# Kernel optimization log

Measured on AMD Instinct MI355X. Metric: run time of the kernel, lower is better.

Reference implementation:

```python
import jax, jax.numpy as jnp
import numpy as np

B, S = 2048, 8192


def setup_inputs() -> dict:
    key = jax.random.key(0)
    ks = jax.random.split(key, 8)
    X = jax.random.normal(ks[0], (B, S, 4), dtype=jnp.float32)
    # make column 0 a monotonically increasing time grid (seconds)
    t = jnp.broadcast_to(jnp.arange(S, dtype=jnp.float32), (B, S))
    X = X.at[..., 0].set(t)
    SC = jax.random.uniform(ks[1], (B, 4), dtype=jnp.float32, minval=0.5, maxval=1.5)
    W1 = jax.random.normal(ks[2], (1, 4), dtype=jnp.float32) * 0.5
    b1 = jnp.zeros((1,), jnp.float32)
    W2 = jax.random.normal(ks[3], (1, 1), dtype=jnp.float32) * 0.5
    b2 = jnp.zeros((1,), jnp.float32)
    Wa = jax.random.normal(ks[4], (1, 2), dtype=jnp.float32) * 0.5
    ba = jnp.zeros((1,), jnp.float32)
    Wb = jax.random.normal(ks[5], (1, 1), dtype=jnp.float32) * 0.5
    bb = jnp.zeros((1,), jnp.float32)
    return {"X": X, "SC": SC, "W1": W1, "b1": b1, "W2": W2, "b2": b2,
            "Wa": Wa, "ba": ba, "Wb": Wb, "bb": bb}


def reference(X, SC, W1, b1, W2, b2, Wa, ba, Wb, bb):
    # X: [B,S,4] = (t, I, T, U); SC: [B,4] = (Q, eta_0, R, SOC_init_ref)
    I = X[..., 1:2]          # [B,S,1]
    T = X[..., 2:3]
    U = X[..., 3:4]
    R = SC[..., 2:3]         # [B,1]
    # initial-SOC net on first-step features
    init_feats = jnp.concatenate(
        [I[:, 0:1], T[:, 0:1], U[:, 0:1], R[:, None, :]], axis=-1)  # [B,1,4]
    h = jax.nn.softplus(init_feats @ W1.T + b1)
    SOC_init_raw = (h @ W2.T + b2).squeeze(-1)                      # [B,1]
    SOC_init = (SC[..., 3:4] * (1.0 + SOC_init_raw))[:, :, None]    # [B,1,1]
    # efficiency-correction net over whole sequence
    eta_in = jnp.concatenate([I, T], axis=-1)                       # [B,S,2]
    delta_eta = jax.nn.softplus(eta_in @ Wa.T + ba) @ Wb.T + bb     # [B,S,1]
    Q = SC[..., 0:1][:, None, :]     # [B,1,1]
    eta0 = SC[..., 1:2][:, None, :]  # [B,1,1]
    # dSOC/dt does not depend on SOC -> Euler loop == prefix sum
    rate = eta0 * (1.0 + delta_eta) * I / (3600.0 * Q)              # [B,S,1]
    times = X[..., 0]                                               # [B,S]
    dt = (times[:, 1:] - times[:, :-1])[..., None]                  # [B,S-1,1]
    delta_SOC = rate[:, :-1] * dt                                   # [B,S-1,1]
    SOC = jnp.concatenate(
        [SOC_init, SOC_init + jnp.cumsum(delta_SOC, axis=1)], axis=1)  # [B,S,1]
    return SOC
```

## Files before the change

### kernel.cpp

```cpp
#include <hip/hip_runtime.h>


#define BLOCK 1024

__device__ __forceinline__ float softplusf(float x) {
    return fmaxf(x, 0.0f) + log1pf(expf(-fabsf(x)));
}

__global__ __launch_bounds__(BLOCK) void soc_scan_kernel(
    const float* __restrict__ X,
    const float* __restrict__ SC,
    const float* __restrict__ W1, const float* __restrict__ b1,
    const float* __restrict__ W2, const float* __restrict__ b2,
    const float* __restrict__ Wa, const float* __restrict__ ba,
    const float* __restrict__ Wb, const float* __restrict__ bb,
    float* __restrict__ out, const int S)
{
    const int b    = blockIdx.x;
    const int tid  = threadIdx.x;
    const int lane = tid & 63;
    const int wv   = tid >> 6;
    const int NW   = BLOCK >> 6;

    __shared__ float sEdgeRate[16];
    __shared__ float sEdgeT[16];
    __shared__ float sWaveSum[16];
    __shared__ float sWaveOff[16];
    __shared__ float sBlockTot;
    __shared__ float sPrevRate;
    __shared__ float sPrevT;

    const float w10 = W1[0], w11 = W1[1], w12 = W1[2], w13 = W1[3];
    const float B1  = b1[0], w2v = W2[0], B2 = b2[0];
    const float wa0 = Wa[0], wa1 = Wa[1], BA = ba[0];
    const float wbv = Wb[0], BB  = bb[0];

    const float Q    = SC[b*4 + 0];
    const float eta0 = SC[b*4 + 1];
    const float Rr   = SC[b*4 + 2];
    const float sc3  = SC[b*4 + 3];

    const float4* __restrict__ Xrow = (const float4*)X + (size_t)b * S;
    float* __restrict__ orow = out + (size_t)b * S;

    float4 x0 = Xrow[0];
    const float h0   = softplusf(x0.y*w10 + x0.z*w11 + x0.w*w12 + Rr*w13 + B1);
    const float soc0 = sc3 * (1.0f + (h0*w2v + B2));
    const float denom = 3600.0f * Q;

    float4 x = Xrow[tid];
    float carry = 0.0f;

    for (int tile = 0; tile < S; tile += BLOCK) {
        const int s = tile + tid;

        const int snext = (tile + BLOCK < S) ? (s + BLOCK) : s;
        float4 xn = Xrow[snext];

        const float t  = x.x;
        const float de   = softplusf(x.y*wa0 + x.z*wa1 + BA) * wbv + BB;
        const float rate = eta0 * (1.0f + de) * x.y / denom;

        if (lane == 63) { sEdgeRate[wv] = rate; sEdgeT[wv] = t; }
        __syncthreads();

        float rp = __shfl_up(rate, 1, 64);
        float tp = __shfl_up(t,    1, 64);
        if (lane == 0) {
            if (wv > 0) { rp = sEdgeRate[wv - 1]; tp = sEdgeT[wv - 1]; }
            else        { rp = sPrevRate;         tp = sPrevT;         }
        }
        const float c = (s == 0) ? 0.0f : rp * (t - tp);

        float v = c;
        #pragma unroll
        for (int off = 1; off < 64; off <<= 1) {
            float n = __shfl_up(v, off, 64);
            if (lane >= off) v += n;
        }
        if (lane == 63) sWaveSum[wv] = v;
        __syncthreads();

        if (wv == 0 && lane < NW) {
            float ws  = sWaveSum[lane];
            float acc = ws;
            #pragma unroll
            for (int off = 1; off < 16; off <<= 1) {
                float n = __shfl_up(acc, off, 64);
                if (lane >= off) acc += n;
            }
            sWaveOff[lane] = acc - ws;
            if (lane == NW - 1) sBlockTot = acc;
        }
        __syncthreads();

        orow[s] = soc0 + carry + sWaveOff[wv] + v;
        carry += sBlockTot;

        if (tid == BLOCK - 1) { sPrevRate = rate; sPrevT = t; }
        x = xn;
    }
}

extern "C" void kernel_launch(void* const* d_in, const int* in_sizes, int n_in,
                              void* d_out, int out_size, void* d_ws, size_t ws_size,
                              hipStream_t stream) {
    const float* X  = (const float*)d_in[0];
    const float* SC = (const float*)d_in[1];
    const float* W1 = (const float*)d_in[2];
    const float* b1 = (const float*)d_in[3];
    const float* W2 = (const float*)d_in[4];
    const float* b2 = (const float*)d_in[5];
    const float* Wa = (const float*)d_in[6];
    const float* ba = (const float*)d_in[7];
    const float* Wb = (const float*)d_in[8];
    const float* bb = (const float*)d_in[9];
    float* out = (float*)d_out;

    const int B = in_sizes[1] / 4;
    const int S = in_sizes[0] / (B * 4);

    soc_scan_kernel<<<B, BLOCK, 0, stream>>>(X, SC, W1, b1, W2, b2,
                                             Wa, ba, Wb, bb, out, S);
}
```

Before: 399.1 us.

## Specialize row scan for S=8192 with all tiles loaded upfront

```diff
diff --git a/kernel.cpp b/kernel.cpp
--- a/kernel.cpp
+++ b/kernel.cpp
@@ -2,14 +2,105 @@
 
 
 #define BLOCK 1024
+#define NT 8
 
 __device__ __forceinline__ float softplusf(float x) {
     return fmaxf(x, 0.0f) + log1pf(expf(-fabsf(x)));
 }
 
-__global__ __launch_bounds__(BLOCK) void soc_scan_kernel(
+__global__ __launch_bounds__(BLOCK) void soc_row_kernel(
     const float* __restrict__ X,
     const float* __restrict__ SC,
+    const float* __restrict__ W1, const float* __restrict__ b1,
+    const float* __restrict__ W2, const float* __restrict__ b2,
+    const float* __restrict__ Wa, const float* __restrict__ ba,
+    const float* __restrict__ Wb, const float* __restrict__ bb,
+    float* __restrict__ out)
+{
+    const int b    = blockIdx.x;
+    const int tid  = threadIdx.x;
+    const int lane = tid & 63;
+    const int wv   = tid >> 6;
+
+    __shared__ float sER[NT][16];
+    __shared__ float sET[NT][16];
+    __shared__ float sWS[NT * 16];
+    __shared__ float sOff[NT * 16];
+
+    const float w10 = W1[0], w11 = W1[1], w12 = W1[2], w13 = W1[3];
+    const float B1  = b1[0], w2v = W2[0], B2 = b2[0];
+    const float wa0 = Wa[0], wa1 = Wa[1], BA = ba[0];
+    const float wbv = Wb[0], BB  = bb[0];
+
+    const float Q    = SC[b*4 + 0];
+    const float eta0 = SC[b*4 + 1];
+    const float Rr   = SC[b*4 + 2];
+    const float sc3  = SC[b*4 + 3];
+    const float denom = 3600.0f * Q;
+
+    const float4* __restrict__ Xrow = (const float4*)X + (size_t)b * (NT * BLOCK);
+    float* __restrict__ orow = out + (size_t)b * (NT * BLOCK);
+
+    float4 x0 = Xrow[0];
+    const float h0   = softplusf(x0.y*w10 + x0.z*w11 + x0.w*w12 + Rr*w13 + B1);
+    const float soc0 = sc3 * (1.0f + (h0*w2v + B2));
+
+    float4 x[NT];
+    #pragma unroll
+    for (int j = 0; j < NT; ++j) x[j] = Xrow[j * BLOCK + tid];
+
+    float rate[NT], tv[NT];
+    #pragma unroll
+    for (int j = 0; j < NT; ++j) {
+        tv[j] = x[j].x;
+        const float de = softplusf(x[j].y*wa0 + x[j].z*wa1 + BA) * wbv + BB;
+        rate[j] = eta0 * (1.0f + de) * x[j].y / denom;
+        if (lane == 63) { sER[j][wv] = rate[j]; sET[j][wv] = tv[j]; }
+    }
+    __syncthreads();
+
+    float v[NT];
+    #pragma unroll
+    for (int j = 0; j < NT; ++j) {
+        float rp = __shfl_up(rate[j], 1, 64);
+        float tp = __shfl_up(tv[j],   1, 64);
+        if (lane == 0) {
+            if (wv > 0)     { rp = sER[j][wv-1]; tp = sET[j][wv-1]; }
+            else if (j > 0) { rp = sER[j-1][15]; tp = sET[j-1][15]; }
+        }
+        float c = rp * (tv[j] - tp);
+        v[j] = c;
+        #pragma unroll
+        for (int off = 1; off < 64; off <<= 1) {
+            float n = __shfl_up(v[j], off, 64);
+            if (lane >= off) v[j] += n;
+        }
+        if (lane == 63) sWS[j * 16 + wv] = v[j];
+    }
+    __syncthreads();
+
+    if (wv == 0) {
+        const float2 p2 = ((const float2*)sWS)[lane];
+        const float p   = p2.x + p2.y;
+        float acc = p;
+        #pragma unroll
+        for (int off = 1; off < 64; off <<= 1) {
+            float n = __shfl_up(acc, off, 64);
+            if (lane >= off) acc += n;
+        }
+        const float excl = acc - p;
+        sOff[2*lane]     = excl;
+        sOff[2*lane + 1] = excl + p2.x;
+    }
+    __syncthreads();
+
+    #pragma unroll
+    for (int j = 0; j < NT; ++j)
+        orow[j * BLOCK + tid] = soc0 + sOff[j * 16 + wv] + v[j];
+}
+
+__global__ __launch_bounds__(BLOCK) void soc_scan_generic(
+    const float* __restrict__ X, const float* __restrict__ SC,
     const float* __restrict__ W1, const float* __restrict__ b1,
     const float* __restrict__ W2, const float* __restrict__ b2,
     const float* __restrict__ Wa, const float* __restrict__ ba,
@@ -22,13 +113,8 @@
     const int wv   = tid >> 6;
     const int NW   = BLOCK >> 6;
 
-    __shared__ float sEdgeRate[16];
-    __shared__ float sEdgeT[16];
-    __shared__ float sWaveSum[16];
-    __shared__ float sWaveOff[16];
-    __shared__ float sBlockTot;
-    __shared__ float sPrevRate;
-    __shared__ float sPrevT;
+    __shared__ float sEdgeRate[16], sEdgeT[16], sWaveSum[16], sWaveOff[16];
+    __shared__ float sBlockTot, sPrevRate, sPrevT;
 
     const float w10 = W1[0], w11 = W1[1], w12 = W1[2], w13 = W1[3];
     const float B1  = b1[0], w2v = W2[0], B2 = b2[0];
@@ -53,11 +139,10 @@
 
     for (int tile = 0; tile < S; tile += BLOCK) {
         const int s = tile + tid;
-
         const int snext = (tile + BLOCK < S) ? (s + BLOCK) : s;
         float4 xn = Xrow[snext];
 
-        const float t  = x.x;
+        const float t    = x.x;
         const float de   = softplusf(x.y*wa0 + x.z*wa1 + BA) * wbv + BB;
         const float rate = eta0 * (1.0f + de) * x.y / denom;
 
@@ -120,6 +205,11 @@
     const int B = in_sizes[1] / 4;
     const int S = in_sizes[0] / (B * 4);
 
-    soc_scan_kernel<<<B, BLOCK, 0, stream>>>(X, SC, W1, b1, W2, b2,
-                                             Wa, ba, Wb, bb, out, S);
-}
+    if (S == NT * BLOCK) {
+        soc_row_kernel<<<B, BLOCK, 0, stream>>>(X, SC, W1, b1, W2, b2,
+                                                Wa, ba, Wb, bb, out);
+    } else {
+        soc_scan_generic<<<B, BLOCK, 0, stream>>>(X, SC, W1, b1, W2, b2,
+                                                  Wa, ba, Wb, bb, out, S);
+    }
+}
```

After: 395.4 us. Within noise of the previous version (-0.9%).
